# Optimization experiments

Hardware: AMD Instinct MI355X
Metric: run time of the kernel (lower is better)

The kernel has to match this reference:

```python
import jax, jax.numpy as jnp
import numpy as np

B, L, S, E, H = 2, 2048, 2048, 1024, 16
D = E // H


def setup_inputs() -> dict:
    key = jax.random.key(0)
    ks = jax.random.split(key, 16)
    p = 0.02  # small init scale for weights
    return {
        "a": jax.random.normal(ks[0], (B, L, E), jnp.float32),
        "b": jax.random.normal(ks[1], (B, S, E), jnp.float32),
        "Wa_qk": jax.random.normal(ks[2], (E, E), jnp.float32) * p,
        "ba_qk": jax.random.normal(ks[3], (E,), jnp.float32) * p,
        "Wa_v": jax.random.normal(ks[4], (E, E), jnp.float32) * p,
        "ba_v": jax.random.normal(ks[5], (E,), jnp.float32) * p,
        "Wb_qk": jax.random.normal(ks[6], (E, E), jnp.float32) * p,
        "bb_qk": jax.random.normal(ks[7], (E,), jnp.float32) * p,
        "Wb_v": jax.random.normal(ks[8], (E, E), jnp.float32) * p,
        "bb_v": jax.random.normal(ks[9], (E,), jnp.float32) * p,
        "Wa_o": jax.random.normal(ks[10], (E, E), jnp.float32) * p,
        "ba_o": jax.random.normal(ks[11], (E,), jnp.float32) * p,
        "Wb_o": jax.random.normal(ks[12], (E, E), jnp.float32) * p,
        "bb_o": jax.random.normal(ks[13], (E,), jnp.float32) * p,
    }


def _heads(x, n, W, bias):
    # x: [B, N, E] -> projected and split to [B, H, N, D]
    y = x @ W + bias
    return y.reshape(B, n, H, D).transpose(0, 2, 1, 3)


def reference(a, b, Wa_qk, ba_qk, Wa_v, ba_v, Wb_qk, bb_qk, Wb_v, bb_v,
              Wa_o, ba_o, Wb_o, bb_o):
    aq = _heads(a, L, Wa_qk, ba_qk)   # [B,H,L,D]
    av = _heads(a, L, Wa_v, ba_v)     # [B,H,L,D]
    bq = _heads(b, S, Wb_qk, bb_qk)   # [B,H,S,D]
    bv = _heads(b, S, Wb_v, bb_v)     # [B,H,S,D]

    scale = 1.0 / jnp.sqrt(jnp.float32(D))
    # Shared score matrix [B,H,L,S]
    scores = jnp.einsum('bhld,bhsd->bhls', aq, bq) * scale
    # Dual softmax: row-wise (over S) and column-wise (over L)
    wa = jax.nn.softmax(scores, axis=-1)                    # [B,H,L,S]
    wb = jax.nn.softmax(scores, axis=-2).transpose(0, 1, 3, 2)  # [B,H,S,L]

    a_ctx = jnp.einsum('bhls,bhsd->bhld', wa, bv)  # [B,H,L,D]
    b_ctx = jnp.einsum('bhsl,bhld->bhsd', wb, av)  # [B,H,S,D]

    a_out = a_ctx.transpose(0, 2, 1, 3).reshape(B, L, E) @ Wa_o + ba_o
    b_out = b_ctx.transpose(0, 2, 1, 3).reshape(B, S, E) @ Wb_o + bb_o
    return (a_out, b_out)
```

## Files before the change

### kernel.cpp

```cpp
#include <hip/hip_runtime.h>
#include <hip/hip_bf16.h>
#include <stdint.h>

typedef unsigned short u16;
typedef unsigned int u32;
typedef __attribute__((ext_vector_type(8))) short bf16x8;
typedef __attribute__((ext_vector_type(4))) float f32x4;

typedef __attribute__((address_space(3))) void lds_void;
typedef const __attribute__((address_space(1))) void gbl_void;

#define SIDE 4194304u
#define BHSTR 131072u

static __device__ __forceinline__ u16 f2bf(float f) {
  union { __hip_bfloat16 b; u16 u; } cv;
  cv.b = __float2bfloat16(f);
  return cv.u;
}
static __device__ __forceinline__ float bf2f(u16 u) {
  union { __hip_bfloat16 b; u16 u; } cv;
  cv.u = u;
  return __bfloat162float(cv.b);
}

static __device__ __forceinline__ float fast_exp2(float x) {
#if __has_builtin(__builtin_amdgcn_exp2f)
  return __builtin_amdgcn_exp2f(x);
#else
  float r;
  asm("v_exp_f32 %0, %1" : "=v"(r) : "v"(x));
  return r;
#endif
}

static __device__ __forceinline__ void pl16swap(u32& a, u32& b) {
#if __has_builtin(__builtin_amdgcn_permlane16_swap)
  typedef __attribute__((ext_vector_type(2))) unsigned int u32x2;
  u32x2 r = __builtin_amdgcn_permlane16_swap(a, b, 0, 0);
  a = r[0];
  b = r[1];
#else
  asm volatile("v_permlane16_swap_b32 %0, %1" : "+v"(a), "+v"(b));
#endif
}

__global__ __launch_bounds__(256) void k_cvt_in(const float* __restrict__ a,
                                                const float* __restrict__ b,
                                                u16* __restrict__ dst) {
  int z = blockIdx.y;
  const float* src = z ? b : a;
  size_t i = ((size_t)blockIdx.x * 256 + threadIdx.x) * 8;
  float4 x0 = *(const float4*)(src + i);
  float4 x1 = *(const float4*)(src + i + 4);
  u16 t[8] = {f2bf(x0.x), f2bf(x0.y), f2bf(x0.z), f2bf(x0.w),
              f2bf(x1.x), f2bf(x1.y), f2bf(x1.z), f2bf(x1.w)};
  *(uint4*)(dst + (size_t)z * SIDE + i) = *(uint4*)t;
}

__global__ __launch_bounds__(256) void k_cvt_bias(
    const float* s0, const float* s1, const float* s2, const float* s3,
    const float* s4, const float* s5, u16* __restrict__ dst) {
  const float* srcs[6] = {s0, s1, s2, s3, s4, s5};
  int z = blockIdx.y;
  int i = blockIdx.x * 256 + threadIdx.x;
  float sc = (z == 0) ? 0.18033688011112042f : 1.0f;
  dst[z * 1024 + i] = f2bf(srcs[z][i] * sc);
}

__global__ __launch_bounds__(256) void k_transpose_w(
    const float* a0, const float* a1, const float* a2, const float* a3,
    const float* a4, const float* a5,
    u16* d0, u16* d1, u16* d2, u16* d3, u16* d4, u16* d5) {
  __shared__ u16 tile[64][72];
  const float* srcs[6] = {a0, a1, a2, a3, a4, a5};
  u16* dsts[6] = {d0, d1, d2, d3, d4, d5};
  int z = blockIdx.z;
  float sc = (z == 0) ? 0.18033688011112042f : 1.0f;
  const float* src = srcs[z] + (size_t)(blockIdx.y * 64) * 1024 + blockIdx.x * 64;
  int t = threadIdx.x;
  int row = t >> 2, c4 = t & 3;
#pragma unroll
  for (int p = 0; p < 2; ++p) {
    int col = c4 * 8 + p * 32;
    const float* sf = src + (size_t)row * 1024 + col;
    float4 x0 = *(const float4*)sf;
    float4 x1 = *(const float4*)(sf + 4);
    u16 tmp[8] = {f2bf(x0.x * sc), f2bf(x0.y * sc), f2bf(x0.z * sc), f2bf(x0.w * sc),
                  f2bf(x1.x * sc), f2bf(x1.y * sc), f2bf(x1.z * sc), f2bf(x1.w * sc)};
    *(uint4*)(&tile[row][col]) = *(uint4*)tmp;
  }
  __syncthreads();
  u16* dst = dsts[z] + (size_t)(blockIdx.x * 64) * 1024 + blockIdx.y * 64;
#pragma unroll
  for (int p = 0; p < 2; ++p) {
    int col = c4 * 8 + p * 32;
    u16 tmp[8];
#pragma unroll
    for (int i = 0; i < 8; ++i) tmp[i] = tile[col + i][row];
    *(uint4*)(dst + (size_t)row * 1024 + col) = *(uint4*)tmp;
  }
}

__global__ __launch_bounds__(256) void k_gemm_qkv(
    const u16* __restrict__ Aall, const u16* __restrict__ WtA,
    const u16* __restrict__ WtB, const u16* __restrict__ bias,
    u16* __restrict__ qkbuf, u16* __restrict__ vtbuf) {
  __shared__ u16 Sh[16384];
  u16* As = Sh;
  u16* Bs = Sh + 8192;
  int tid = threadIdx.x;
  int wave = tid >> 6, lane = tid & 63;
  int quad = lane >> 4, lrow = lane & 15;
  int wr = wave >> 1, wc = wave & 1;
  int lin = blockIdx.x + 16 * blockIdx.y + 512 * blockIdx.z;
  int s = (lin & 7) * 128 + (lin >> 3);
  int bx = s & 15, by = (s >> 4) & 31, bz = s >> 9;
  int z = bz;
  int m0 = by * 128, n0 = bx * 128;
  const u16* A = Aall + (size_t)z * SIDE;
  const u16* Wt = z ? WtB : WtA;
  const u16* bi = bias + (size_t)z * 2048;

  f32x4 acc[4][4] = {};
  int srow = 32 * wave + (lane >> 3);
  int ssw = ((lane & 7) ^ (lane >> 3)) * 8;
  const u16* gA = A + (size_t)(m0 + srow) * 1024 + ssw;
  const u16* gB = Wt + (size_t)(n0 + srow) * 1024 + ssw;
  u16* lA = &As[(32 * wave) * 64];
  u16* lB = &Bs[(32 * wave) * 64];

  for (int k0 = 0; k0 < 1024; k0 += 64) {
    __syncthreads();
#pragma unroll
    for (int j = 0; j < 4; ++j) {
      __builtin_amdgcn_global_load_lds((gbl_void*)(gA + (size_t)(8 * j) * 1024 + k0),
                                       (lds_void*)(lA + 8 * j * 64), 16, 0, 0);
      __builtin_amdgcn_global_load_lds((gbl_void*)(gB + (size_t)(8 * j) * 1024 + k0),
                                       (lds_void*)(lB + 8 * j * 64), 16, 0, 0);
    }
    __syncthreads();
#pragma unroll
    for (int kk = 0; kk < 2; ++kk) {
      int gq = ((kk << 2) + quad) ^ (lrow & 7);
      bf16x8 af[4], bfr[4];
#pragma unroll
      for (int i = 0; i < 4; ++i)
        af[i] = *(const bf16x8*)&As[(64 * wr + 16 * i + lrow) * 64 + gq * 8];
#pragma unroll
      for (int j = 0; j < 4; ++j)
        bfr[j] = *(const bf16x8*)&Bs[(64 * wc + 16 * j + lrow) * 64 + gq * 8];
#pragma unroll
      for (int i = 0; i < 4; ++i)
#pragma unroll
        for (int j = 0; j < 4; ++j)
          acc[i][j] = __builtin_amdgcn_mfma_f32_16x16x32_bf16(af[i], bfr[j], acc[i][j], 0, 0, 0);
    }
  }

  float bv[4];
#pragma unroll
  for (int j = 0; j < 4; ++j) bv[j] = bf2f(bi[n0 + 64 * wc + 16 * j + lrow]);

  bool isv = (bx >= 8);
  int h = (isv ? 2 * (bx - 8) : 2 * bx) + wc;

  __syncthreads();

  if (isv) {
    u16* Vw = Sh + wave * 4096;
    int rg0 = m0 + 64 * wr;
    int bb = rg0 >> 11, rl0 = rg0 & 2047;
#pragma unroll
    for (int i = 0; i < 4; ++i)
#pragma unroll
      for (int j = 0; j < 4; ++j) {
        int d = 16 * j + lrow;
        int gw = (2 * i + (quad >> 1)) ^ (d & 7);
        u16 tmp[4];
#pragma unroll
        for (int r = 0; r < 4; ++r) tmp[r] = f2bf(acc[i][j][r] + bv[j]);
        *(uint2*)&Vw[d * 64 + (gw << 3) + 4 * (quad & 1)] = *(uint2*)tmp;
      }
    asm volatile("s_waitcnt lgkmcnt(0)" ::: "memory");
    u16* vdst = vtbuf + (size_t)z * SIDE + (size_t)(bb * 16 + h) * BHSTR + rl0;
#pragma unroll
    for (int p = 0; p < 8; ++p) {
      int d = 8 * p + (lane >> 3);
      int gr = (lane & 7) ^ (d & 7);
      uint4 q = *(const uint4*)&Vw[d * 64 + (gr << 3)];
      *(uint4*)(vdst + (size_t)d * 2048 + (lane & 7) * 8) = q;
    }
  } else {
    u16* dst = qkbuf + (size_t)z * SIDE;
    u16* lw = Sh + wave * 1216;
#pragma unroll
    for (int i = 0; i < 4; ++i) {
#pragma unroll
      for (int j = 0; j < 4; ++j)
#pragma unroll
        for (int r = 0; r < 4; ++r)
          lw[(4 * quad + r) * 76 + 16 * j + lrow] = f2bf(acc[i][j][r] + bv[j]);
      asm volatile("s_waitcnt lgkmcnt(0)" ::: "memory");
      int row = lane >> 2, cg = (lane & 3) * 16;
      int rg = m0 + 64 * wr + 16 * i + row;
      int bb = rg >> 11, rl = rg & 2047;
      u16* dr = dst + (size_t)(bb * 16 + h) * BHSTR + (size_t)rl * 64 + cg;
      uint2 w0 = *(const uint2*)&lw[row * 76 + cg];
      uint2 w1 = *(const uint2*)&lw[row * 76 + cg + 4];
      uint2 w2 = *(const uint2*)&lw[row * 76 + cg + 8];
      uint2 w3 = *(const uint2*)&lw[row * 76 + cg + 12];
      uint4 o0 = {w0.x, w0.y, w1.x, w1.y};
      uint4 o1 = {w2.x, w2.y, w3.x, w3.y};
      *(uint4*)dr = o0;
      *(uint4*)(dr + 8) = o1;
      asm volatile("s_waitcnt lgkmcnt(0)" ::: "memory");
    }
  }
}

__global__ __launch_bounds__(256, 4) void k_attn(
    const u16* __restrict__ qk, const u16* __restrict__ vt,
    u16* __restrict__ ctx) {
  __shared__ u16 Ks[2 * 4096];
  __shared__ u16 Vs[2 * 4096];
  int tid = threadIdx.x;
  int wave = tid >> 6, lane = tid & 63;
  int quad = lane >> 4, lrow = lane & 15;
  int z = blockIdx.z, bh = blockIdx.x;
  int l0 = blockIdx.y * 128;
  const u16* Qb = qk + (size_t)z * SIDE + (size_t)bh * BHSTR + (size_t)l0 * 64;
  const u16* Kb = qk + (size_t)(1 - z) * SIDE + (size_t)bh * BHSTR;
  const u16* Vtb = vt + (size_t)(1 - z) * SIDE + (size_t)bh * BHSTR;

  bf16x8 qf[2][2];
#pragma unroll
  for (int rt = 0; rt < 2; ++rt) {
    int lq = 32 * wave + 16 * rt + lrow;
    qf[rt][0] = *(const bf16x8*)&Qb[(size_t)lq * 64 + 8 * quad];
    qf[rt][1] = *(const bf16x8*)&Qb[(size_t)lq * 64 + 32 + 8 * quad];
  }

  int r0 = tid >> 3, c0 = tid & 7;
  int r1 = (256 + tid) >> 3;
  const u16* kS0 = Kb + (size_t)r0 * 64 + ((c0 ^ (r0 & 7)) * 8);
  const u16* kS1 = Kb + (size_t)r1 * 64 + ((c0 ^ (r1 & 7)) * 8);
  const u16* vS0 = Vtb + (size_t)r0 * 2048 + ((c0 ^ (r0 & 7)) * 8);
  const u16* vS1 = Vtb + (size_t)r1 * 2048 + ((c0 ^ (r1 & 7)) * 8);
  u16* kD0 = Ks + (wave * 64) * 8;
  u16* kD1 = Ks + (256 + wave * 64) * 8;
  u16* vD0 = Vs + (wave * 64) * 8;
  u16* vD1 = Vs + (256 + wave * 64) * 8;

  bf16x8 ones;
  {
    short o = 0x3F80;
#pragma unroll
    for (int i = 0; i < 8; ++i) ones[i] = o;
  }

  f32x4 cacc[2][4] = {};
  f32x4 asum[2] = {};
  int gsq = 2 * (quad & 1) + (quad >> 1);

#define STAGE(BUFOFF, IT)                                                        \
  __builtin_amdgcn_global_load_lds((gbl_void*)(kS0 + (size_t)(IT)*4096),         \
                                   (lds_void*)(kD0 + (BUFOFF)), 16, 0, 0);       \
  __builtin_amdgcn_global_load_lds((gbl_void*)(kS1 + (size_t)(IT)*4096),         \
                                   (lds_void*)(kD1 + (BUFOFF)), 16, 0, 0);       \
  __builtin_amdgcn_global_load_lds((gbl_void*)(vS0 + (size_t)(IT)*64),           \
                                   (lds_void*)(vD0 + (BUFOFF)), 16, 0, 0);       \
  __builtin_amdgcn_global_load_lds((gbl_void*)(vS1 + (size_t)(IT)*64),           \
                                   (lds_void*)(vD1 + (BUFOFF)), 16, 0, 0);

#define ATT_BODY(BUFOFF)                                                         \
  {                                                                              \
    const u16* KsC = Ks + (BUFOFF);                                              \
    const u16* VsC = Vs + (BUFOFF);                                              \
    u32 X[2][4], Y[2][4];                                                        \
    _Pragma("unroll") for (int j = 0; j < 4; ++j) {                              \
      int kr = 16 * j + lrow;                                                    \
      bf16x8 kf0 = *(const bf16x8*)&KsC[(kr * 8 + (quad ^ (kr & 7))) * 8];       \
      bf16x8 kf1 = *(const bf16x8*)&KsC[(kr * 8 + ((quad + 4) ^ (kr & 7))) * 8]; \
      _Pragma("unroll") for (int rt = 0; rt < 2; ++rt) {                         \
        f32x4 s = {};                                                            \
        s = __builtin_amdgcn_mfma_f32_16x16x32_bf16(kf0, qf[rt][0], s, 0, 0, 0); \
        s = __builtin_amdgcn_mfma_f32_16x16x32_bf16(kf1, qf[rt][1], s, 0, 0, 0); \
        float e0 = fast_exp2(s[0]), e1 = fast_exp2(s[1]);                        \
        float e2 = fast_exp2(s[2]), e3 = fast_exp2(s[3]);                        \
        X[rt][j] = ((u32)f2bf(e1) << 16) | (u32)f2bf(e0);                        \
        Y[rt][j] = ((u32)f2bf(e3) << 16) | (u32)f2bf(e2);                        \
      }                                                                          \
    }                                                                            \
    bf16x8 pf[2][2];                                                             \
    _Pragma("unroll") for (int rt = 0; rt < 2; ++rt) {                           \
      pl16swap(X[rt][0], X[rt][1]);                                              \
      pl16swap(Y[rt][0], Y[rt][1]);                                              \
      pl16swap(X[rt][2], X[rt][3]);                                              \
      pl16swap(Y[rt][2], Y[rt][3]);                                              \
      union { u32 d[4]; bf16x8 v; } u0, u1;                                      \
      u0.d[0] = X[rt][0]; u0.d[1] = Y[rt][0];                                    \
      u0.d[2] = X[rt][1]; u0.d[3] = Y[rt][1];                                    \
      u1.d[0] = X[rt][2]; u1.d[1] = Y[rt][2];                                    \
      u1.d[2] = X[rt][3]; u1.d[3] = Y[rt][3];                                    \
      pf[rt][0] = u0.v;                                                          \
      pf[rt][1] = u1.v;                                                          \
    }                                                                            \
    __builtin_amdgcn_s_setprio(1);                                               \
    _Pragma("unroll") for (int jd = 0; jd < 4; ++jd) {                           \
      int vr = 16 * jd + lrow;                                                   \
      bf16x8 vf0 = *(const bf16x8*)&VsC[(vr * 8 + (gsq ^ (vr & 7))) * 8];        \
      bf16x8 vf1 = *(const bf16x8*)&VsC[(vr * 8 + ((gsq | 4) ^ (vr & 7))) * 8];  \
      _Pragma("unroll") for (int rt = 0; rt < 2; ++rt) {                         \
        cacc[rt][jd] = __builtin_amdgcn_mfma_f32_16x16x32_bf16(pf[rt][0], vf0, cacc[rt][jd], 0, 0, 0); \
        cacc[rt][jd] = __builtin_amdgcn_mfma_f32_16x16x32_bf16(pf[rt][1], vf1, cacc[rt][jd], 0, 0, 0); \
      }                                                                          \
    }                                                                            \
    _Pragma("unroll") for (int rt = 0; rt < 2; ++rt) {                           \
      asum[rt] = __builtin_amdgcn_mfma_f32_16x16x32_bf16(pf[rt][0], ones, asum[rt], 0, 0, 0); \
      asum[rt] = __builtin_amdgcn_mfma_f32_16x16x32_bf16(pf[rt][1], ones, asum[rt], 0, 0, 0); \
    }                                                                            \
    __builtin_amdgcn_s_setprio(0);                                               \
  }

  STAGE(0, 0)

  for (int it2 = 0; it2 < 16; ++it2) {
    int it = 2 * it2;
    __syncthreads();
    STAGE(4096, it + 1)
    ATT_BODY(0)
    __syncthreads();
    if (it2 < 15) {
      STAGE(0, it + 2)
    }
    ATT_BODY(4096)
  }
#undef ATT_BODY
#undef STAGE

  int bb = bh >> 4, h = bh & 15;
  u16* Ob = ctx + (size_t)z * SIDE + (size_t)(bb * 2048 + l0) * 1024 + h * 64;
#pragma unroll
  for (int rt = 0; rt < 2; ++rt) {
#pragma unroll
    for (int r = 0; r < 4; ++r) {
      float rinv = 1.0f / asum[rt][r];
      int l = 32 * wave + 16 * rt + 4 * quad + r;
#pragma unroll
      for (int j = 0; j < 4; ++j)
        Ob[(size_t)l * 1024 + 16 * j + lrow] = f2bf(cacc[rt][j][r] * rinv);
    }
  }
}

__global__ __launch_bounds__(256) void k_gemm_o(
    const u16* __restrict__ ctx, const u16* __restrict__ WtO,
    const u16* __restrict__ bias, float* __restrict__ out) {
  __shared__ u16 As[128 * 64];
  __shared__ u16 Bs[128 * 64];
  int tid = threadIdx.x;
  int wave = tid >> 6, lane = tid & 63;
  int quad = lane >> 4, lrow = lane & 15;
  int wr = wave >> 1, wc = wave & 1;
  int lin = blockIdx.x + 8 * blockIdx.y + 256 * blockIdx.z;
  int s = (lin & 7) * 64 + (lin >> 3);
  int bx = s & 7, by = (s >> 3) & 31, bz = s >> 8;
  int z = bz;
  int m0 = by * 128, n0 = bx * 128;
  const u16* A = ctx + (size_t)z * SIDE;
  const u16* Wt = WtO + (size_t)z * 1048576;
  const u16* bi = bias + (size_t)z * 1024;
  float* C = out + (size_t)z * SIDE;

  f32x4 acc[4][4] = {};
  int srow = 32 * wave + (lane >> 3);
  int ssw = ((lane & 7) ^ (lane >> 3)) * 8;
  const u16* gA = A + (size_t)(m0 + srow) * 1024 + ssw;
  const u16* gB = Wt + (size_t)(n0 + srow) * 1024 + ssw;
  u16* lA = &As[(32 * wave) * 64];
  u16* lB = &Bs[(32 * wave) * 64];

  for (int k0 = 0; k0 < 1024; k0 += 64) {
    __syncthreads();
#pragma unroll
    for (int j = 0; j < 4; ++j) {
      __builtin_amdgcn_global_load_lds((gbl_void*)(gA + (size_t)(8 * j) * 1024 + k0),
                                       (lds_void*)(lA + 8 * j * 64), 16, 0, 0);
      __builtin_amdgcn_global_load_lds((gbl_void*)(gB + (size_t)(8 * j) * 1024 + k0),
                                       (lds_void*)(lB + 8 * j * 64), 16, 0, 0);
    }
    __syncthreads();
#pragma unroll
    for (int kk = 0; kk < 2; ++kk) {
      int gq = ((kk << 2) + quad) ^ (lrow & 7);
      bf16x8 af[4], bfr[4];
#pragma unroll
      for (int i = 0; i < 4; ++i)
        af[i] = *(const bf16x8*)&As[(64 * wr + 16 * i + lrow) * 64 + gq * 8];
#pragma unroll
      for (int j = 0; j < 4; ++j)
        bfr[j] = *(const bf16x8*)&Bs[(64 * wc + 16 * j + lrow) * 64 + gq * 8];
#pragma unroll
      for (int i = 0; i < 4; ++i)
#pragma unroll
        for (int j = 0; j < 4; ++j)
          acc[i][j] = __builtin_amdgcn_mfma_f32_16x16x32_bf16(af[i], bfr[j], acc[i][j], 0, 0, 0);
    }
  }

  float bv[4];
#pragma unroll
  for (int j = 0; j < 4; ++j) bv[j] = bf2f(bi[n0 + 64 * wc + 16 * j + lrow]);
#pragma unroll
  for (int i = 0; i < 4; ++i) {
    int row = m0 + 64 * wr + 16 * i + 4 * quad;
#pragma unroll
    for (int j = 0; j < 4; ++j) {
      int col = n0 + 64 * wc + 16 * j + lrow;
#pragma unroll
      for (int r = 0; r < 4; ++r)
        C[(size_t)(row + r) * 1024 + col] = acc[i][j][r] + bv[j];
    }
  }
}

extern "C" void kernel_launch(void* const* d_in, const int* in_sizes, int n_in,
                              void* d_out, int out_size, void* d_ws, size_t ws_size,
                              hipStream_t stream) {
  (void)in_sizes; (void)n_in; (void)out_size; (void)ws_size;
  const size_t M1 = 1048576u;
  u16* ws = (u16*)d_ws;
  u16* wtA   = ws;
  u16* wtB   = ws + 2 * M1;
  u16* wtO   = ws + 4 * M1;
  u16* biasQ = ws + 6 * M1;
  u16* biasO = ws + 6 * M1 + 4096;
  u16* ab    = ws + 7 * M1;
  u16* ctx   = ab;
  u16* qkbuf = ws + 15 * M1;
  u16* vt    = ws + 23 * M1;

  dim3 blk(256);
  k_cvt_in<<<dim3(2048, 2), blk, 0, stream>>>((const float*)d_in[0],
                                              (const float*)d_in[1], ab);
  k_cvt_bias<<<dim3(4, 6), blk, 0, stream>>>(
      (const float*)d_in[3], (const float*)d_in[5], (const float*)d_in[7],
      (const float*)d_in[9], (const float*)d_in[11], (const float*)d_in[13], biasQ);
  k_transpose_w<<<dim3(16, 16, 6), blk, 0, stream>>>(
      (const float*)d_in[2], (const float*)d_in[4], (const float*)d_in[6],
      (const float*)d_in[8], (const float*)d_in[10], (const float*)d_in[12],
      wtA, wtA + M1, wtB, wtB + M1, wtO, wtO + M1);
  k_gemm_qkv<<<dim3(16, 32, 2), blk, 0, stream>>>(ab, wtA, wtB, biasQ, qkbuf, vt);
  k_attn<<<dim3(32, 16, 2), blk, 0, stream>>>(qkbuf, vt, ctx);
  k_gemm_o<<<dim3(8, 32, 2), blk, 0, stream>>>(ctx, wtO, biasO, (float*)d_out);
}
```

Measured before the change: 262.2 us.

## Double-buffer LDS tiles in QKV and output projection GEMMs

Both projection GEMM kernels now use two LDS buffers and issue the async global-to-LDS loads for the next K tile before computing on the current one, with one barrier per half-step instead of two per step. This is meant to hide global load latency behind the MFMA work. LDS per block doubles to 64 KB, which may reduce occupancy. The extra barrier before the V epilogue is dropped because the loop now ends on a sync.

Measured after the change: 263.9 us. Within noise of the previous version (+0.6%).

```diff
diff --git a/kernel.cpp b/kernel.cpp
--- a/kernel.cpp
+++ b/kernel.cpp
@@ -106,9 +106,7 @@
     const u16* __restrict__ Aall, const u16* __restrict__ WtA,
     const u16* __restrict__ WtB, const u16* __restrict__ bias,
     u16* __restrict__ qkbuf, u16* __restrict__ vtbuf) {
-  __shared__ u16 Sh[16384];
-  u16* As = Sh;
-  u16* Bs = Sh + 8192;
+  __shared__ u16 Sh[32768];
   int tid = threadIdx.x;
   int wave = tid >> 6, lane = tid & 63;
   int quad = lane >> 4, lrow = lane & 15;
@@ -127,36 +125,46 @@
   int ssw = ((lane & 7) ^ (lane >> 3)) * 8;
   const u16* gA = A + (size_t)(m0 + srow) * 1024 + ssw;
   const u16* gB = Wt + (size_t)(n0 + srow) * 1024 + ssw;
-  u16* lA = &As[(32 * wave) * 64];
-  u16* lB = &Bs[(32 * wave) * 64];
-
-  for (int k0 = 0; k0 < 1024; k0 += 64) {
-    __syncthreads();
-#pragma unroll
-    for (int j = 0; j < 4; ++j) {
-      __builtin_amdgcn_global_load_lds((gbl_void*)(gA + (size_t)(8 * j) * 1024 + k0),
-                                       (lds_void*)(lA + 8 * j * 64), 16, 0, 0);
-      __builtin_amdgcn_global_load_lds((gbl_void*)(gB + (size_t)(8 * j) * 1024 + k0),
-                                       (lds_void*)(lB + 8 * j * 64), 16, 0, 0);
-    }
-    __syncthreads();
-#pragma unroll
-    for (int kk = 0; kk < 2; ++kk) {
-      int gq = ((kk << 2) + quad) ^ (lrow & 7);
-      bf16x8 af[4], bfr[4];
-#pragma unroll
-      for (int i = 0; i < 4; ++i)
-        af[i] = *(const bf16x8*)&As[(64 * wr + 16 * i + lrow) * 64 + gq * 8];
-#pragma unroll
-      for (int j = 0; j < 4; ++j)
-        bfr[j] = *(const bf16x8*)&Bs[(64 * wc + 16 * j + lrow) * 64 + gq * 8];
-#pragma unroll
-      for (int i = 0; i < 4; ++i)
-#pragma unroll
-        for (int j = 0; j < 4; ++j)
-          acc[i][j] = __builtin_amdgcn_mfma_f32_16x16x32_bf16(af[i], bfr[j], acc[i][j], 0, 0, 0);
-    }
-  }
+
+#define STG(B, K0)                                                               \
+  _Pragma("unroll") for (int j = 0; j < 4; ++j) {                                \
+    __builtin_amdgcn_global_load_lds(                                            \
+        (gbl_void*)(gA + (size_t)(8 * j) * 1024 + (K0)),                         \
+        (lds_void*)(Sh + (B)*16384 + wave * 2048 + j * 512), 16, 0, 0);          \
+    __builtin_amdgcn_global_load_lds(                                            \
+        (gbl_void*)(gB + (size_t)(8 * j) * 1024 + (K0)),                         \
+        (lds_void*)(Sh + (B)*16384 + 8192 + wave * 2048 + j * 512), 16, 0, 0);   \
+  }
+
+#define CMP(B)                                                                   \
+  _Pragma("unroll") for (int kk = 0; kk < 2; ++kk) {                             \
+    int gq = ((kk << 2) + quad) ^ (lrow & 7);                                    \
+    bf16x8 af[4], bfr[4];                                                        \
+    _Pragma("unroll") for (int i = 0; i < 4; ++i)                                \
+      af[i] = *(const bf16x8*)&Sh[(B)*16384 + (64 * wr + 16 * i + lrow) * 64 + gq * 8]; \
+    _Pragma("unroll") for (int j = 0; j < 4; ++j)                                \
+      bfr[j] = *(const bf16x8*)&Sh[(B)*16384 + 8192 + (64 * wc + 16 * j + lrow) * 64 + gq * 8]; \
+    _Pragma("unroll") for (int i = 0; i < 4; ++i)                                \
+      _Pragma("unroll") for (int j = 0; j < 4; ++j)                              \
+        acc[i][j] = __builtin_amdgcn_mfma_f32_16x16x32_bf16(af[i], bfr[j], acc[i][j], 0, 0, 0); \
+  }
+
+  STG(0, 0)
+  __syncthreads();
+#pragma unroll 1
+  for (int it2 = 0; it2 < 8; ++it2) {
+    int k0 = it2 * 128;
+    STG(1, k0 + 64)
+    CMP(0)
+    __syncthreads();
+    if (it2 < 7) {
+      STG(0, k0 + 128)
+    }
+    CMP(1)
+    __syncthreads();
+  }
+#undef STG
+#undef CMP
 
   float bv[4];
 #pragma unroll
@@ -164,8 +172,6 @@
 
   bool isv = (bx >= 8);
   int h = (isv ? 2 * (bx - 8) : 2 * bx) + wc;
-
-  __syncthreads();
 
   if (isv) {
     u16* Vw = Sh + wave * 4096;
@@ -357,8 +363,7 @@
 __global__ __launch_bounds__(256) void k_gemm_o(
     const u16* __restrict__ ctx, const u16* __restrict__ WtO,
     const u16* __restrict__ bias, float* __restrict__ out) {
-  __shared__ u16 As[128 * 64];
-  __shared__ u16 Bs[128 * 64];
+  __shared__ u16 Sh[32768];
   int tid = threadIdx.x;
   int wave = tid >> 6, lane = tid & 63;
   int quad = lane >> 4, lrow = lane & 15;
@@ -378,36 +383,46 @@
   int ssw = ((lane & 7) ^ (lane >> 3)) * 8;
   const u16* gA = A + (size_t)(m0 + srow) * 1024 + ssw;
   const u16* gB = Wt + (size_t)(n0 + srow) * 1024 + ssw;
-  u16* lA = &As[(32 * wave) * 64];
-  u16* lB = &Bs[(32 * wave) * 64];
-
-  for (int k0 = 0; k0 < 1024; k0 += 64) {
-    __syncthreads();
-#pragma unroll
-    for (int j = 0; j < 4; ++j) {
-      __builtin_amdgcn_global_load_lds((gbl_void*)(gA + (size_t)(8 * j) * 1024 + k0),
-                                       (lds_void*)(lA + 8 * j * 64), 16, 0, 0);
-      __builtin_amdgcn_global_load_lds((gbl_void*)(gB + (size_t)(8 * j) * 1024 + k0),
-                                       (lds_void*)(lB + 8 * j * 64), 16, 0, 0);
-    }
-    __syncthreads();
-#pragma unroll
-    for (int kk = 0; kk < 2; ++kk) {
-      int gq = ((kk << 2) + quad) ^ (lrow & 7);
-      bf16x8 af[4], bfr[4];
-#pragma unroll
-      for (int i = 0; i < 4; ++i)
-        af[i] = *(const bf16x8*)&As[(64 * wr + 16 * i + lrow) * 64 + gq * 8];
-#pragma unroll
-      for (int j = 0; j < 4; ++j)
-        bfr[j] = *(const bf16x8*)&Bs[(64 * wc + 16 * j + lrow) * 64 + gq * 8];
-#pragma unroll
-      for (int i = 0; i < 4; ++i)
-#pragma unroll
-        for (int j = 0; j < 4; ++j)
-          acc[i][j] = __builtin_amdgcn_mfma_f32_16x16x32_bf16(af[i], bfr[j], acc[i][j], 0, 0, 0);
-    }
-  }
+
+#define STG(B, K0)                                                               \
+  _Pragma("unroll") for (int j = 0; j < 4; ++j) {                                \
+    __builtin_amdgcn_global_load_lds(                                            \
+        (gbl_void*)(gA + (size_t)(8 * j) * 1024 + (K0)),                         \
+        (lds_void*)(Sh + (B)*16384 + wave * 2048 + j * 512), 16, 0, 0);          \
+    __builtin_amdgcn_global_load_lds(                                            \
+        (gbl_void*)(gB + (size_t)(8 * j) * 1024 + (K0)),                         \
+        (lds_void*)(Sh + (B)*16384 + 8192 + wave * 2048 + j * 512), 16, 0, 0);   \
+  }
+
+#define CMP(B)                                                                   \
+  _Pragma("unroll") for (int kk = 0; kk < 2; ++kk) {                             \
+    int gq = ((kk << 2) + quad) ^ (lrow & 7);                                    \
+    bf16x8 af[4], bfr[4];                                                        \
+    _Pragma("unroll") for (int i = 0; i < 4; ++i)                                \
+      af[i] = *(const bf16x8*)&Sh[(B)*16384 + (64 * wr + 16 * i + lrow) * 64 + gq * 8]; \
+    _Pragma("unroll") for (int j = 0; j < 4; ++j)                                \
+      bfr[j] = *(const bf16x8*)&Sh[(B)*16384 + 8192 + (64 * wc + 16 * j + lrow) * 64 + gq * 8]; \
+    _Pragma("unroll") for (int i = 0; i < 4; ++i)                                \
+      _Pragma("unroll") for (int j = 0; j < 4; ++j)                              \
+        acc[i][j] = __builtin_amdgcn_mfma_f32_16x16x32_bf16(af[i], bfr[j], acc[i][j], 0, 0, 0); \
+  }
+
+  STG(0, 0)
+  __syncthreads();
+#pragma unroll 1
+  for (int it2 = 0; it2 < 8; ++it2) {
+    int k0 = it2 * 128;
+    STG(1, k0 + 64)
+    CMP(0)
+    __syncthreads();
+    if (it2 < 7) {
+      STG(0, k0 + 128)
+    }
+    CMP(1)
+    __syncthreads();
+  }
+#undef STG
+#undef CMP
 
   float bv[4];
 #pragma unroll
```
